# Kernel optimization log

Measured on AMD Instinct MI355X. Metric: run time of the kernel, lower is better.

## Reference

```python
import jax, jax.numpy as jnp
import numpy as np

B, CIN, COUT, COFF, H, W = 4, 256, 256, 256, 64, 64
DG, K = 16, 3            # deformable groups, kernel size
KK = K * K               # 9 taps


def _conv3x3(x, w, b):
    y = jax.lax.conv_general_dilated(x, w, window_strides=(1, 1), padding='SAME',
                                     dimension_numbers=('NCHW', 'OIHW', 'NCHW'))
    return y + b[None, :, None, None]


def _bilinear_sample(xg, ys, xs):
    # xg: [B,DG,Cg,H,W]; ys,xs: [B,DG,Ho,Wo] float sampling coords (zero padding outside)
    Bn, dg, Cg, Hh, Ww = xg.shape
    xf = xg.reshape(Bn, dg, Cg, Hh * Ww)
    y0 = jnp.floor(ys)
    x0 = jnp.floor(xs)
    wy = (ys - y0)[:, :, None]  # [B,DG,1,Ho,Wo]
    wx = (xs - x0)[:, :, None]

    def gather(yi, xi):
        valid = (yi >= 0) & (yi < Hh) & (xi >= 0) & (xi < Ww)
        yc = jnp.clip(yi, 0, Hh - 1).astype(jnp.int32)
        xc = jnp.clip(xi, 0, Ww - 1).astype(jnp.int32)
        idx = (yc * Ww + xc).reshape(Bn, dg, 1, -1)
        v = jnp.take_along_axis(xf, jnp.broadcast_to(idx, (Bn, dg, Cg, idx.shape[-1])), axis=-1)
        v = v.reshape(Bn, dg, Cg, ys.shape[2], ys.shape[3])
        return v * valid[:, :, None].astype(xg.dtype)

    v00 = gather(y0, x0)
    v01 = gather(y0, x0 + 1)
    v10 = gather(y0 + 1, x0)
    v11 = gather(y0 + 1, x0 + 1)
    return v00 * (1 - wy) * (1 - wx) + v01 * (1 - wy) * wx + v10 * wy * (1 - wx) + v11 * wy * wx


def _deform_conv2d(x, offset, mask, weight, bias):
    # torchvision modulated deform_conv2d, stride=1, padding=1, dilation=1, groups=1
    Bn, C, Hh, Ww = x.shape
    Cg = C // DG
    xg = x.reshape(Bn, DG, Cg, Hh, Ww)
    # offset channel layout: 2*(g*KK + k) -> dy, +1 -> dx
    off = offset.reshape(Bn, DG, KK, 2, Hh, Ww)
    msk = mask.reshape(Bn, DG, KK, Hh, Ww)
    wk = weight.reshape(weight.shape[0], DG, Cg, K, K)
    hb = jnp.arange(Hh, dtype=x.dtype)[:, None]
    wb = jnp.arange(Ww, dtype=x.dtype)[None, :]
    acc = jnp.zeros((Bn, weight.shape[0], Hh, Ww), dtype=x.dtype)
    for ki in range(K):
        for kj in range(K):
            k = ki * K + kj
            ys = hb - 1 + ki + off[:, :, k, 0]   # padding=1, dilation=1
            xs = wb - 1 + kj + off[:, :, k, 1]
            s = _bilinear_sample(xg, ys, xs) * msk[:, :, k][:, :, None]  # [B,DG,Cg,H,W]
            acc = acc + jnp.einsum('bgchw,ogc->bohw', s, wk[:, :, :, ki, kj])
    return acc + bias[None, :, None, None]


def setup_inputs() -> dict:
    key = jax.random.key(0)
    ks = jax.random.split(key, 10)
    s = 0.02
    return {
        'x': jax.random.normal(ks[0], (B, CIN, H, W), jnp.float32),
        'offset_feat': jax.random.normal(ks[1], (B, COFF, H, W), jnp.float32),
        'weight': jax.random.normal(ks[2], (COUT, CIN, K, K), jnp.float32) * s,
        'bias': jax.random.normal(ks[3], (COUT,), jnp.float32) * s,
        'w1': jax.random.normal(ks[4], (COUT, COFF, K, K), jnp.float32) * s,
        'b1': jax.random.normal(ks[5], (COUT,), jnp.float32) * s,
        'w2': jax.random.normal(ks[6], (COUT, COUT, K, K), jnp.float32) * s,
        'b2': jax.random.normal(ks[7], (COUT,), jnp.float32) * s,
        'w3': jax.random.normal(ks[8], (27 * DG, COUT, K, K), jnp.float32) * 0.01,
        'b3': jax.random.normal(ks[9], (27 * DG,), jnp.float32) * 0.01,
    }


def reference(x, offset_feat, weight, bias, w1, b1, w2, b2, w3, b3):
    out = jax.nn.silu(_conv3x3(offset_feat, w1, b1))
    out = jax.nn.silu(_conv3x3(out, w2, b2))
    out = _conv3x3(out, w3, b3)                 # [B, 27*DG, H, W]
    o1, o2, m = jnp.split(out, 3, axis=1)
    offset = jnp.concatenate([o1, o2], axis=1)  # [B, 2*DG*9, H, W]
    mask = jax.nn.sigmoid(m)                    # [B, DG*9, H, W]
    return _deform_conv2d(x, offset, mask, weight, bias)
```

## Files before the change

kernel.cpp:

```cpp
#include <hip/hip_runtime.h>
#include <math.h>

typedef __attribute__((ext_vector_type(8))) short  bf16x8;
typedef __attribute__((ext_vector_type(8))) unsigned short u16x8;
typedef __attribute__((ext_vector_type(4))) float  f32x4;

__device__ __forceinline__ float b2f(unsigned short h) {
  return __uint_as_float(((unsigned int)h) << 16);
}
__device__ __forceinline__ unsigned short f2bf(float f) {
  unsigned int u = __float_as_uint(f);
  unsigned int r = (u + 0x7fffu + ((u >> 16) & 1u)) >> 16;
  return (unsigned short)r;
}
__device__ __forceinline__ void gload16(const unsigned short* g, unsigned short* l) {
  __builtin_amdgcn_global_load_lds(
      (const __attribute__((address_space(1))) void*)g,
      (__attribute__((address_space(3))) void*)l, 16, 0, 0);
}

__global__ __launch_bounds__(256) void nhwc_kernel(const float* __restrict__ in,
                                                   unsigned short* __restrict__ out) {
  const int y = blockIdx.x, b = blockIdx.y;
  const int t = threadIdx.x;
  __shared__ float lds[64 * 65];
  for (int c0 = 0; c0 < 256; c0 += 64) {
    #pragma unroll
    for (int i = 0; i < 16; ++i) {
      int cl = i * 4 + (t >> 6);
      int xx = t & 63;
      lds[cl * 65 + xx] = in[(((size_t)b * 256 + c0 + cl) * 64 + y) * 64 + xx];
    }
    __syncthreads();
    #pragma unroll
    for (int i = 0; i < 16; ++i) {
      int xx = i * 4 + (t >> 6);
      int cl = t & 63;
      out[(((size_t)b * 64 + y) * 64 + xx) * 256 + c0 + cl] = f2bf(lds[cl * 65 + xx]);
    }
    __syncthreads();
  }
}

__global__ __launch_bounds__(256) void wprep_kernel(const float* __restrict__ w,
                                                    unsigned short* __restrict__ Wp,
                                                    int COUT_valid) {
  const int kk = blockIdx.x;
  const int co = blockIdx.y;
  const int ci = threadIdx.x;
  float v = (co < COUT_valid) ? w[((size_t)co * 256 + ci) * 9 + kk] : 0.0f;
  Wp[(size_t)co * 2304 + kk * 256 + ci] = f2bf(v);
}

__global__ __launch_bounds__(256) void sampler_kernel(const float* __restrict__ t3,
                                                      const unsigned short* __restrict__ xh,
                                                      unsigned short* __restrict__ S) {
  const int t = threadIdx.x;
  const int g = t & 15;
  const int m = blockIdx.x * 16 + (t >> 4);
  const int b = m >> 12, pix = m & 4095, y = pix >> 6, x = pix & 63;
  const float* off = t3 + (size_t)m * 432;

  #pragma unroll
  for (int kk = 0; kk < 9; ++kk) {
    const int ki = kk / 3, kj = kk % 3;
    float dyv = off[2 * (g * 9 + kk)];
    float dxv = off[2 * (g * 9 + kk) + 1];
    float ml  = off[288 + g * 9 + kk];
    float mk  = 1.0f / (1.0f + __expf(-ml));
    float ysf = (float)(y - 1 + ki) + dyv;
    float xsf = (float)(x - 1 + kj) + dxv;
    float y0f = floorf(ysf), x0f = floorf(xsf);
    float wy = ysf - y0f, wx = xsf - x0f;
    int yi0 = (int)y0f, xi0 = (int)x0f;
    int yi1 = yi0 + 1, xi1 = xi0 + 1;
    bool vy0 = (yi0 >= 0) && (yi0 < 64), vy1 = (yi1 >= 0) && (yi1 < 64);
    bool vx0 = (xi0 >= 0) && (xi0 < 64), vx1 = (xi1 >= 0) && (xi1 < 64);
    int yc0 = min(max(yi0, 0), 63), yc1 = min(max(yi1, 0), 63);
    int xc0 = min(max(xi0, 0), 63), xc1 = min(max(xi1, 0), 63);
    float w00 = (vy0 && vx0) ? (1.f - wy) * (1.f - wx) * mk : 0.f;
    float w01 = (vy0 && vx1) ? (1.f - wy) * wx * mk : 0.f;
    float w10 = (vy1 && vx0) ? wy * (1.f - wx) * mk : 0.f;
    float w11 = (vy1 && vx1) ? wy * wx * mk : 0.f;

    float sacc[16];
    #pragma unroll
    for (int c = 0; c < 16; ++c) sacc[c] = 0.f;

    const size_t bbase = (size_t)(b << 12) * 256 + g * 16;
    const int p00 = yc0 * 64 + xc0, p01 = yc0 * 64 + xc1;
    const int p10 = yc1 * 64 + xc0, p11 = yc1 * 64 + xc1;
    {
      u16x8 lo = *(const u16x8*)(xh + bbase + (size_t)p00 * 256);
      u16x8 hi = *(const u16x8*)(xh + bbase + (size_t)p00 * 256 + 8);
      #pragma unroll
      for (int j = 0; j < 8; ++j) { sacc[j] += w00 * b2f(lo[j]); sacc[8 + j] += w00 * b2f(hi[j]); }
    }
    {
      u16x8 lo = *(const u16x8*)(xh + bbase + (size_t)p01 * 256);
      u16x8 hi = *(const u16x8*)(xh + bbase + (size_t)p01 * 256 + 8);
      #pragma unroll
      for (int j = 0; j < 8; ++j) { sacc[j] += w01 * b2f(lo[j]); sacc[8 + j] += w01 * b2f(hi[j]); }
    }
    {
      u16x8 lo = *(const u16x8*)(xh + bbase + (size_t)p10 * 256);
      u16x8 hi = *(const u16x8*)(xh + bbase + (size_t)p10 * 256 + 8);
      #pragma unroll
      for (int j = 0; j < 8; ++j) { sacc[j] += w10 * b2f(lo[j]); sacc[8 + j] += w10 * b2f(hi[j]); }
    }
    {
      u16x8 lo = *(const u16x8*)(xh + bbase + (size_t)p11 * 256);
      u16x8 hi = *(const u16x8*)(xh + bbase + (size_t)p11 * 256 + 8);
      #pragma unroll
      for (int j = 0; j < 8; ++j) { sacc[j] += w11 * b2f(lo[j]); sacc[8 + j] += w11 * b2f(hi[j]); }
    }
    u16x8 olo, ohi;
    #pragma unroll
    for (int j = 0; j < 8; ++j) { olo[j] = f2bf(sacc[j]); ohi[j] = f2bf(sacc[8 + j]); }
    unsigned short* sp = S + (size_t)m * 2304 + kk * 256 + g * 16;
    *(u16x8*)sp = olo;
    *(u16x8*)(sp + 8) = ohi;
  }
}

template<int EPI, bool IMPLICIT>
__global__ __launch_bounds__(256, 2) void gemm_kernel(
    const unsigned short* __restrict__ A,
    const unsigned short* __restrict__ W,
    const float* __restrict__ bias,
    void* __restrict__ outp,
    const unsigned short* __restrict__ zbuf,
    int K, int Nvalid) {
  constexpr int BM = 128, BN = 64, BK = 64;
  constexpr int NSTEP = 36;
  constexpr int BUFE = (BM + BN) * BK;
  __shared__ unsigned short lds[3][BUFE];

  const int t = threadIdx.x, lane = t & 63, w = t >> 6;
  const int wm = w >> 1, wn = w & 1;
  const int m0 = blockIdx.x * BM, n0 = blockIdx.y * BN;

  const unsigned short* baseA[4];
  const unsigned short* zsrcA[4];
  unsigned int vmaskA[4];
  #pragma unroll
  for (int i = 0; i < 4; ++i) {
    int c   = (i * 4 + w) * 64 + lane;
    int row = c >> 3;
    int ccl = (c & 7) ^ (row & 7);
    int m   = m0 + row;
    if (IMPLICIT) {
      int y = (m >> 6) & 63, x = m & 63;
      unsigned int vm = 0;
      #pragma unroll
      for (int kk = 0; kk < 9; ++kk) {
        int dy = kk / 3 - 1, dx = kk % 3 - 1;
        if ((unsigned)(y + dy) < 64u && (unsigned)(x + dx) < 64u) vm |= (1u << kk);
      }
      vmaskA[i] = vm;
      baseA[i] = A + (size_t)m * 256 + ccl * 8;
      zsrcA[i] = zbuf + ccl * 8;
    } else {
      baseA[i] = A + (size_t)m * K + ccl * 8;
      zsrcA[i] = zbuf;
      vmaskA[i] = 0;
    }
  }
  const unsigned short* baseB[2];
  #pragma unroll
  for (int j = 0; j < 2; ++j) {
    int c   = (16 + j * 4 + w) * 64 + lane;
    int row = (c - 1024) >> 3;
    int ccl = (c & 7) ^ (row & 7);
    baseB[j] = W + (size_t)(n0 + row) * K + ccl * 8;
  }

  int offA[4][2], offB[2][2];
  #pragma unroll
  for (int mi = 0; mi < 4; ++mi) {
    int r = wm * 64 + mi * 16 + (lane & 15);
    #pragma unroll
    for (int kh = 0; kh < 2; ++kh) {
      int ccl = kh * 4 + (lane >> 4);
      offA[mi][kh] = r * 64 + ((ccl ^ (r & 7)) * 8);
    }
  }
  #pragma unroll
  for (int nj = 0; nj < 2; ++nj) {
    int r = wn * 32 + nj * 16 + (lane & 15);
    #pragma unroll
    for (int kh = 0; kh < 2; ++kh) {
      int ccl = kh * 4 + (lane >> 4);
      offB[nj][kh] = BM * BK + r * 64 + ((ccl ^ (r & 7)) * 8);
    }
  }

  f32x4 acc[4][2];
  #pragma unroll
  for (int mi = 0; mi < 4; ++mi)
    #pragma unroll
    for (int nj = 0; nj < 2; ++nj) acc[mi][nj] = (f32x4){0.f, 0.f, 0.f, 0.f};

  auto STAGE = [&](int sn, unsigned short* buf) {
    if (IMPLICIT) {
      int kkn = sn >> 2;
      int ci0 = (sn & 3) * 64;
      int q3  = kkn / 3;
      int soff = ((q3 - 1) * 64 + (kkn - q3 * 3 - 1)) * 256 + ci0;
      #pragma unroll
      for (int i = 0; i < 4; ++i) {
        const unsigned short* src = ((vmaskA[i] >> kkn) & 1u) ? baseA[i] + soff : zsrcA[i];
        gload16(src, buf + (i * 4 + w) * 512);
      }
    } else {
      #pragma unroll
      for (int i = 0; i < 4; ++i)
        gload16(baseA[i] + (size_t)sn * 64, buf + (i * 4 + w) * 512);
    }
    #pragma unroll
    for (int j = 0; j < 2; ++j)
      gload16(baseB[j] + (size_t)sn * 64, buf + 8192 + (j * 4 + w) * 512);
  };

  STAGE(0, lds[0]);
  STAGE(1, lds[1]);

  int cur = 0, nxt2 = 2;
  for (int s = 0; s < NSTEP; ++s) {
    __builtin_amdgcn_sched_barrier(0);
    if (s < NSTEP - 1) {
      asm volatile("s_waitcnt vmcnt(6)" ::: "memory");
    } else {
      asm volatile("s_waitcnt vmcnt(0)" ::: "memory");
    }
    __builtin_amdgcn_s_barrier();
    __builtin_amdgcn_sched_barrier(0);

    if (s + 2 < NSTEP) STAGE(s + 2, lds[nxt2]);

    const unsigned short* cb = lds[cur];
    bf16x8 af[4][2], bfg[2][2];
    #pragma unroll
    for (int mi = 0; mi < 4; ++mi)
      #pragma unroll
      for (int kh = 0; kh < 2; ++kh)
        af[mi][kh] = *(const bf16x8*)&cb[offA[mi][kh]];
    #pragma unroll
    for (int nj = 0; nj < 2; ++nj)
      #pragma unroll
      for (int kh = 0; kh < 2; ++kh)
        bfg[nj][kh] = *(const bf16x8*)&cb[offB[nj][kh]];

    #pragma unroll
    for (int kh = 0; kh < 2; ++kh)
      #pragma unroll
      for (int mi = 0; mi < 4; ++mi)
        #pragma unroll
        for (int nj = 0; nj < 2; ++nj)
          acc[mi][nj] = __builtin_amdgcn_mfma_f32_16x16x32_bf16(af[mi][kh], bfg[nj][kh],
                                                                acc[mi][nj], 0, 0, 0);
    cur = (cur == 2) ? 0 : cur + 1;
    nxt2 = (nxt2 == 2) ? 0 : nxt2 + 1;
  }

  const int gmBase = m0 + wm * 64 + (lane >> 4) * 4;
  const int gnBase = n0 + wn * 32 + (lane & 15);
  #pragma unroll
  for (int nj = 0; nj < 2; ++nj) {
    const int gn = gnBase + nj * 16;
    const float bv = (gn < Nvalid) ? bias[gn] : 0.f;
    #pragma unroll
    for (int mi = 0; mi < 4; ++mi) {
      #pragma unroll
      for (int r = 0; r < 4; ++r) {
        const int gm = gmBase + mi * 16 + r;
        float v = acc[mi][nj][r] + bv;
        if (EPI == 0) {
          float sv = v / (1.0f + __expf(-v));
          ((unsigned short*)outp)[(size_t)gm * 256 + gn] = f2bf(sv);
        } else if (EPI == 1) {
          if (gn < Nvalid) ((float*)outp)[(size_t)gm * 432 + gn] = v;
        } else {
          ((float*)outp)[((size_t)(gm >> 12) * 256 + gn) * 4096 + (gm & 4095)] = v;
        }
      }
    }
  }
}

extern "C" void kernel_launch(void* const* d_in, const int* in_sizes, int n_in,
                              void* d_out, int out_size, void* d_ws, size_t ws_size,
                              hipStream_t stream) {
  const float* x      = (const float*)d_in[0];
  const float* offeat = (const float*)d_in[1];
  const float* weight = (const float*)d_in[2];
  const float* bias   = (const float*)d_in[3];
  const float* w1     = (const float*)d_in[4];
  const float* b1     = (const float*)d_in[5];
  const float* w2     = (const float*)d_in[6];
  const float* b2     = (const float*)d_in[7];
  const float* w3     = (const float*)d_in[8];
  const float* b3     = (const float*)d_in[9];
  float* out = (float*)d_out;

  char* ws = (char*)d_ws;
  unsigned short* xh  = (unsigned short*)(ws + 0);
  float*          t3  = (float*)(ws + 8388608);
  unsigned short* Wd  = (unsigned short*)(ws + 36700160);
  unsigned short* zb  = (unsigned short*)(ws + 37879808);
  unsigned short* S   = (unsigned short*)(ws + 37880064);
  unsigned short* fh  = (unsigned short*)(ws + 37880064);
  unsigned short* t1  = (unsigned short*)(ws + 46268672);
  unsigned short* t2  = (unsigned short*)(ws + 54657280);
  unsigned short* W1p = (unsigned short*)(ws + 63045888);
  unsigned short* W2p = (unsigned short*)(ws + 64225536);
  unsigned short* W3p = (unsigned short*)(ws + 65405184);

  hipMemsetAsync(zb, 0, 256, stream);

  nhwc_kernel<<<dim3(64, 4), 256, 0, stream>>>(x, xh);
  nhwc_kernel<<<dim3(64, 4), 256, 0, stream>>>(offeat, fh);
  wprep_kernel<<<dim3(9, 256), 256, 0, stream>>>(w1, W1p, 256);
  wprep_kernel<<<dim3(9, 256), 256, 0, stream>>>(w2, W2p, 256);
  wprep_kernel<<<dim3(9, 448), 256, 0, stream>>>(w3, W3p, 432);
  wprep_kernel<<<dim3(9, 256), 256, 0, stream>>>(weight, Wd, 256);

  gemm_kernel<0, true><<<dim3(128, 4), 256, 0, stream>>>(fh, W1p, b1, t1, zb, 2304, 256);
  gemm_kernel<0, true><<<dim3(128, 4), 256, 0, stream>>>(t1, W2p, b2, t2, zb, 2304, 256);
  gemm_kernel<1, true><<<dim3(128, 7), 256, 0, stream>>>(t2, W3p, b3, t3, zb, 2304, 432);

  sampler_kernel<<<dim3(1024), 256, 0, stream>>>(t3, xh, S);
  gemm_kernel<2, false><<<dim3(128, 4), 256, 0, stream>>>(S, Wd, bias, out, zb, 2304, 256);
}
```

Before: 210.1 us.

## Split GEMM k-step into two halves with interleaved prefetch and setprio

Result: slower. 219.2 us (+4.3%).

```diff
diff --git a/kernel.cpp b/kernel.cpp
--- a/kernel.cpp
+++ b/kernel.cpp
@@ -201,64 +201,68 @@
     #pragma unroll
     for (int nj = 0; nj < 2; ++nj) acc[mi][nj] = (f32x4){0.f, 0.f, 0.f, 0.f};
 
-  auto STAGE = [&](int sn, unsigned short* buf) {
+  auto STAGE_HALF = [&](int sn, unsigned short* buf, int half) {
+    const int i0 = half * 2;
     if (IMPLICIT) {
       int kkn = sn >> 2;
       int ci0 = (sn & 3) * 64;
       int q3  = kkn / 3;
       int soff = ((q3 - 1) * 64 + (kkn - q3 * 3 - 1)) * 256 + ci0;
       #pragma unroll
-      for (int i = 0; i < 4; ++i) {
+      for (int i = i0; i < i0 + 2; ++i) {
         const unsigned short* src = ((vmaskA[i] >> kkn) & 1u) ? baseA[i] + soff : zsrcA[i];
         gload16(src, buf + (i * 4 + w) * 512);
       }
     } else {
       #pragma unroll
-      for (int i = 0; i < 4; ++i)
+      for (int i = i0; i < i0 + 2; ++i)
         gload16(baseA[i] + (size_t)sn * 64, buf + (i * 4 + w) * 512);
     }
-    #pragma unroll
-    for (int j = 0; j < 2; ++j)
-      gload16(baseB[j] + (size_t)sn * 64, buf + 8192 + (j * 4 + w) * 512);
+    const int j = half;
+    gload16(baseB[j] + (size_t)sn * 64, buf + 8192 + (j * 4 + w) * 512);
   };
 
-  STAGE(0, lds[0]);
-  STAGE(1, lds[1]);
+  STAGE_HALF(0, lds[0], 0); STAGE_HALF(0, lds[0], 1);
+  STAGE_HALF(1, lds[1], 0); STAGE_HALF(1, lds[1], 1);
+  asm volatile("s_waitcnt vmcnt(6)" ::: "memory");
+  __builtin_amdgcn_s_barrier();
 
   int cur = 0, nxt2 = 2;
   for (int s = 0; s < NSTEP; ++s) {
-    __builtin_amdgcn_sched_barrier(0);
-    if (s < NSTEP - 1) {
-      asm volatile("s_waitcnt vmcnt(6)" ::: "memory");
-    } else {
-      asm volatile("s_waitcnt vmcnt(0)" ::: "memory");
-    }
-    __builtin_amdgcn_s_barrier();
-    __builtin_amdgcn_sched_barrier(0);
-
-    if (s + 2 < NSTEP) STAGE(s + 2, lds[nxt2]);
-
     const unsigned short* cb = lds[cur];
-    bf16x8 af[4][2], bfg[2][2];
-    #pragma unroll
-    for (int mi = 0; mi < 4; ++mi)
-      #pragma unroll
-      for (int kh = 0; kh < 2; ++kh)
-        af[mi][kh] = *(const bf16x8*)&cb[offA[mi][kh]];
-    #pragma unroll
-    for (int nj = 0; nj < 2; ++nj)
-      #pragma unroll
-      for (int kh = 0; kh < 2; ++kh)
-        bfg[nj][kh] = *(const bf16x8*)&cb[offB[nj][kh]];
-
-    #pragma unroll
-    for (int kh = 0; kh < 2; ++kh)
+    const bool prefetch = (s + 2 < NSTEP);
+
+    #pragma unroll
+    for (int kh = 0; kh < 2; ++kh) {
+      bf16x8 af[4], bfg[2];
+      #pragma unroll
+      for (int mi = 0; mi < 4; ++mi) af[mi] = *(const bf16x8*)&cb[offA[mi][kh]];
+      #pragma unroll
+      for (int nj = 0; nj < 2; ++nj) bfg[nj] = *(const bf16x8*)&cb[offB[nj][kh]];
+
+      if (prefetch) STAGE_HALF(s + 2, lds[nxt2], kh);
+
+      if (kh == 1) {
+        if (prefetch) asm volatile("s_waitcnt vmcnt(6)" ::: "memory");
+        else          asm volatile("s_waitcnt vmcnt(0)" ::: "memory");
+      }
+      __builtin_amdgcn_sched_barrier(0);
+      __builtin_amdgcn_s_barrier();
+      asm volatile("s_waitcnt lgkmcnt(0)" ::: "memory");
+      __builtin_amdgcn_sched_barrier(0);
+
+      __builtin_amdgcn_s_setprio(1);
       #pragma unroll
       for (int mi = 0; mi < 4; ++mi)
         #pragma unroll
         for (int nj = 0; nj < 2; ++nj)
-          acc[mi][nj] = __builtin_amdgcn_mfma_f32_16x16x32_bf16(af[mi][kh], bfg[nj][kh],
+          acc[mi][nj] = __builtin_amdgcn_mfma_f32_16x16x32_bf16(af[mi], bfg[nj],
                                                                 acc[mi][nj], 0, 0, 0);
+      __builtin_amdgcn_s_setprio(0);
+      __builtin_amdgcn_sched_barrier(0);
+      __builtin_amdgcn_s_barrier();
+    }
+
     cur = (cur == 2) ? 0 : cur + 1;
     nxt2 = (nxt2 == 2) ? 0 : nxt2 + 1;
   }
```
